# Performance work log

Hardware: AMD Instinct MI355X
Metric: run time of the kernel (lower is better)

The kernel has to match this reference:

```python
import jax, jax.numpy as jnp
import numpy as np

ATT_DIM = 2048
NUM_HEADS = 16
NUM_KV_GROUPS = 4
HEAD_DIM = 128
CONTEXT_LENGTH = 2048
ROPE_BASE = 10000.0
GROUP_SIZE = NUM_HEADS // NUM_KV_GROUPS
BATCH = 2


def _precompute_rope_sin(context_length, head_dim, rope_base):
    # thetas over rope_dim = head_dim // 2, exponent uses rope_dim (as in source)
    rope_dim = head_dim // 2
    j = jnp.arange(rope_dim, dtype=jnp.float32)
    thetas = 1.0 / rope_base ** (2.0 * j / rope_dim)
    positions = jnp.arange(context_length, dtype=jnp.float32)
    angles = positions[:, None] * thetas[None, :]          # [CD, HD//2]
    angles = jnp.concatenate([angles, angles], axis=-1)    # [CD, HD]
    return jnp.sin(angles)                                  # cos is unused (see bug note)


def _apply_rope(qk, sin):
    # FAITHFUL to source bug: in compute_rope, `cos` is overwritten with the
    # broadcast `sin`, so the returned value is qk*sin + qk_2*sin.
    hd = qk.shape[-1]
    qkr = qk[..., : hd // 2]
    qki = qk[..., hd // 2 :]
    qk2 = jnp.concatenate([-qki, qkr], axis=-1)
    sin_b = sin[None, None, : qk.shape[2], :]
    return qk * sin_b + qk2 * sin  # second term broadcasts full-length sin (requires cd==context_length)


def setup_inputs() -> dict:
    key = jax.random.key(0)
    ks = jax.random.split(key, 6)
    s = 0.02
    x = jax.random.normal(ks[0], (BATCH, CONTEXT_LENGTH, ATT_DIM), dtype=jnp.float32)
    Wq = jax.random.normal(ks[1], (ATT_DIM, HEAD_DIM * NUM_HEADS), dtype=jnp.float32) * s
    Wk = jax.random.normal(ks[2], (ATT_DIM, HEAD_DIM * NUM_KV_GROUPS), dtype=jnp.float32) * s
    Wv = jax.random.normal(ks[3], (ATT_DIM, HEAD_DIM * NUM_KV_GROUPS), dtype=jnp.float32) * s
    Wo = jax.random.normal(ks[4], (HEAD_DIM * NUM_HEADS, HEAD_DIM * NUM_HEADS), dtype=jnp.float32) * s
    bo = jax.random.normal(ks[5], (HEAD_DIM * NUM_HEADS,), dtype=jnp.float32) * s
    return {"x": x, "Wq": Wq, "Wk": Wk, "Wv": Wv, "Wo": Wo, "bo": bo}


def reference(x, Wq, Wk, Wv, Wo, bo):
    bd, cd, ed = x.shape
    sin = _precompute_rope_sin(CONTEXT_LENGTH, HEAD_DIM, ROPE_BASE)

    q = (x @ Wq).reshape(bd, cd, NUM_HEADS, HEAD_DIM).transpose(0, 2, 1, 3)      # [B,NH,CD,HD]
    k = (x @ Wk).reshape(bd, cd, NUM_KV_GROUPS, HEAD_DIM).transpose(0, 2, 1, 3)  # [B,Nkv,CD,HD]
    v = (x @ Wv).reshape(bd, cd, NUM_KV_GROUPS, HEAD_DIM).transpose(0, 2, 1, 3)

    q = _apply_rope(q, sin)
    k = _apply_rope(k, sin)

    k = jnp.repeat(k, GROUP_SIZE, axis=1)  # [B,NH,CD,HD]
    v = jnp.repeat(v, GROUP_SIZE, axis=1)

    a = jnp.einsum("bhqd,bhkd->bhqk", q, k)  # [B,NH,CD,CD]
    causal = jnp.triu(jnp.ones((cd, cd), dtype=bool), k=1)
    a = jnp.where(causal[None, None], -jnp.inf, a)
    a = jax.nn.softmax(a / jnp.sqrt(jnp.float32(HEAD_DIM)), axis=-1)

    y = jnp.einsum("bhqk,bhkd->bhqd", a, v)                # [B,NH,CD,HD]
    y = y.transpose(0, 2, 1, 3).reshape(bd, cd, HEAD_DIM * NUM_HEADS)
    return y @ Wo + bo
```

## Files before the change

### kernel.cpp

```cpp
#include <hip/hip_runtime.h>
#include <hip/hip_bf16.h>
#include <cstdint>
#include <cstddef>

#define BATCH 2
#define CTX 2048
#define EMB 2048
#define NH 16
#define NG 4
#define HD 128
#define NQK (EMB + 2*NG*HD)
#define MROWS (BATCH*CTX)

typedef __bf16 bf16x8 __attribute__((ext_vector_type(8)));
typedef float  f32x4  __attribute__((ext_vector_type(4)));
typedef float  f32x16 __attribute__((ext_vector_type(16)));

__device__ __forceinline__ ushort f2bf(float f) {
    uint32_t u = __float_as_uint(f);
    u += 0x7FFFu + ((u >> 16) & 1u);
    return (ushort)(u >> 16);
}

__device__ __forceinline__ float bf2f(ushort u) {
    return __uint_as_float((uint32_t)u << 16);
}

__device__ __forceinline__ uint32_t packbf(float a, float b) {
    ushort lo = __builtin_bit_cast(ushort, (__bf16)a);
    ushort hi = __builtin_bit_cast(ushort, (__bf16)b);
    return (uint32_t)lo | ((uint32_t)hi << 16);
}

__device__ __forceinline__ bf16x8 mkfrag(uint32_t a, uint32_t b, uint32_t c, uint32_t d) {
    union { uint32_t u[4]; bf16x8 v; } z;
    z.u[0] = a; z.u[1] = b; z.u[2] = c; z.u[3] = d;
    return z.v;
}

__device__ __forceinline__ void gload_lds16(const void* g, void* l) {
    __builtin_amdgcn_global_load_lds((const __attribute__((address_space(1))) void*)g,
                                     (__attribute__((address_space(3))) void*)l, 16, 0, 0);
}

__global__ __launch_bounds__(256) void k_sintab(float* __restrict__ sintab) {
    int t = blockIdx.x * 256 + threadIdx.x;
    int j = t & 63, p = t >> 6;
    float theta = 1.0f / powf(10000.0f, (float)(2 * j) / 64.0f);
    sintab[t] = sinf((float)p * theta);
}

__global__ __launch_bounds__(256) void k_cvt(const float4* __restrict__ src, ushort4* __restrict__ dst) {
    int i = blockIdx.x * 256 + threadIdx.x;
    float4 v = src[i];
    ushort4 o;
    o.x = f2bf(v.x); o.y = f2bf(v.y); o.z = f2bf(v.z); o.w = f2bf(v.w);
    dst[i] = o;
}

__global__ __launch_bounds__(256) void k_transpose_cvt(const float* __restrict__ src, int src_ld,
                                                       ushort* __restrict__ dst, int dst_ld) {
    __shared__ float tile[32][33];
    int tx = threadIdx.x, ty = threadIdx.y;
    int c0 = blockIdx.x * 32, r0 = blockIdx.y * 32;
    #pragma unroll
    for (int i = 0; i < 4; ++i)
        tile[ty + i*8][tx] = src[(size_t)(r0 + ty + i*8) * src_ld + c0 + tx];
    __syncthreads();
    #pragma unroll
    for (int i = 0; i < 4; ++i)
        dst[(size_t)(c0 + ty + i*8) * dst_ld + r0 + tx] = f2bf(tile[tx][ty + i*8]);
}

__global__ __launch_bounds__(256) void k_rope_f(const ushort* __restrict__ qkv,
                                                const float* __restrict__ sintab,
                                                ushort* __restrict__ Qf, ushort* __restrict__ Kf,
                                                float qs) {
    int t = blockIdx.x * 256 + threadIdx.x;
    int j = t & 63;
    int rest = t >> 6;
    int pos = rest & (CTX - 1);
    int rest2 = rest >> 11;
    int u = rest2 % (NH + NG);
    int b = rest2 / (NH + NG);
    const ushort* base;
    ushort* dst;
    float scale;
    if (u < NH) {
        base = qkv + (size_t)(b * CTX + pos) * NQK + u * HD;
        dst = Qf + (size_t)((b * NH + u) * 64 + (pos >> 5)) * 4096;
        scale = qs;
    } else {
        int g = u - NH;
        base = qkv + (size_t)(b * CTX + pos) * NQK + EMB + g * HD;
        dst = Kf + (size_t)((b * NG + g) * 64 + (pos >> 5)) * 4096;
        scale = 1.0f;
    }
    float a  = bf2f(base[j]);
    float bb = bf2f(base[j + 64]);
    float sv = sintab[pos * 64 + j] * scale;
    size_t idx0 = (size_t)(j >> 4) * 512 + ((j >> 3) & 1) * 256 + (pos & 31) * 8 + (j & 7);
    dst[idx0]        = f2bf((a - bb) * sv);
    dst[idx0 + 2048] = f2bf((bb + a) * sv);
}

__global__ __launch_bounds__(256) void k_vfrag(const ushort* __restrict__ qkvb, ushort* __restrict__ Vf) {
    int lane = threadIdx.x;
    int dt   = threadIdx.y;
    int step = blockIdx.x;
    int bg   = blockIdx.y;
    int b = bg >> 2, g = bg & 3;
    int ln = lane & 31, hi = lane >> 5;
    int col = EMB + NG*HD + g*HD + dt*32 + ln;
    #pragma unroll
    for (int ks = 0; ks < 2; ++ks) {
        int pos0 = step*32 + ks*16 + hi*8;
        ushort v[8];
        #pragma unroll
        for (int e = 0; e < 8; ++e)
            v[e] = qkvb[(size_t)(b*CTX + pos0 + e) * NQK + col];
        union { uint32_t u[4]; bf16x8 bv; } z;
        z.u[0] = (uint32_t)v[0] | ((uint32_t)v[1] << 16);
        z.u[1] = (uint32_t)v[2] | ((uint32_t)v[3] << 16);
        z.u[2] = (uint32_t)v[4] | ((uint32_t)v[5] << 16);
        z.u[3] = (uint32_t)v[6] | ((uint32_t)v[7] << 16);
        *(bf16x8*)(Vf + ((size_t)(bg*64 + step)*8 + dt*2 + ks) * 512 + lane*8) = z.bv;
    }
}

template<bool BF16OUT>
__global__ __launch_bounds__(256) void k_gemm_bt(const ushort* __restrict__ A, const ushort* __restrict__ Bt,
                                                 void* __restrict__ Cv, int M, int N, int K,
                                                 const float* __restrict__ bias) {
    __shared__ __align__(16) ushort As[2][128 * 32];
    __shared__ __align__(16) ushort Bs[2][128 * 32];
    int tid = threadIdx.x;
    int lane = tid & 63;
    int wave = tid >> 6;
    int wr = wave >> 1, wc = wave & 1;
    int m0 = blockIdx.y * 128, n0 = blockIdx.x * 128;
    int lr = lane & 15, lg = lane >> 4;

    f32x4 acc[4][4] = {};

    int arow = lane >> 2;
    int kpart = (lane & 3) * 8;

    int nsteps = K >> 5;

    #pragma unroll
    for (int s = 0; s < 2; ++s) {
        int c = wave * 2 + s;
        gload_lds16(A  + (size_t)(m0 + c*16 + arow) * K + kpart, &As[0][c * 512]);
        gload_lds16(Bt + (size_t)(n0 + c*16 + arow) * K + kpart, &Bs[0][c * 512]);
    }
    __syncthreads();

    for (int t = 0; t < nsteps; ++t) {
        int cur = t & 1;
        if (t + 1 < nsteps) {
            int k1 = (t + 1) << 5;
            #pragma unroll
            for (int s = 0; s < 2; ++s) {
                int c = wave * 2 + s;
                gload_lds16(A  + (size_t)(m0 + c*16 + arow) * K + k1 + kpart, &As[cur ^ 1][c * 512]);
                gload_lds16(Bt + (size_t)(n0 + c*16 + arow) * K + k1 + kpart, &Bs[cur ^ 1][c * 512]);
            }
        }
        bf16x8 af[4], bfr[4];
        #pragma unroll
        for (int mt = 0; mt < 4; ++mt)
            af[mt] = *(const bf16x8*)&As[cur][(wr*64 + mt*16 + lr) * 32 + lg * 8];
        #pragma unroll
        for (int nt = 0; nt < 4; ++nt)
            bfr[nt] = *(const bf16x8*)&Bs[cur][(wc*64 + nt*16 + lr) * 32 + lg * 8];
        #pragma unroll
        for (int mt = 0; mt < 4; ++mt)
            #pragma unroll
            for (int nt = 0; nt < 4; ++nt)
                acc[mt][nt] = __builtin_amdgcn_mfma_f32_16x16x32_bf16(af[mt], bfr[nt], acc[mt][nt], 0, 0, 0);
        __syncthreads();
    }

    #pragma unroll
    for (int mt = 0; mt < 4; ++mt) {
        #pragma unroll
        for (int nt = 0; nt < 4; ++nt) {
            int col = n0 + wc*64 + nt*16 + lr;
            float bv = bias ? bias[col] : 0.0f;
            #pragma unroll
            for (int r = 0; r < 4; ++r) {
                int row = m0 + wr*64 + mt*16 + lg*4 + r;
                float v = acc[mt][nt][r] + bv;
                if constexpr (BF16OUT)
                    ((ushort*)Cv)[(size_t)row * N + col] = f2bf(v);
                else
                    ((float*)Cv)[(size_t)row * N + col] = v;
            }
        }
    }
}

__global__ __launch_bounds__(128) void k_attn12(const ushort* __restrict__ Qf, const ushort* __restrict__ Kf,
                                                const ushort* __restrict__ Vf, ushort* __restrict__ y) {
    __shared__ __align__(16) char smem[16640];
    char*  Qs  = smem;
    float* sOd = (float*)smem;
    float* sl  = (float*)(smem + 16384);

    int lane = threadIdx.x & 63;
    int w    = threadIdx.x >> 6;
    int B  = blockIdx.x;
    int bg = B & 7;
    int within = B >> 3;
    int t  = 63 - (within >> 2);
    int hh = within & 3;
    int b = bg >> 2, g = bg & 3, h = g * 4 + hh;
    int ln = lane & 31, hi = lane >> 5;
    int q0 = t * 32;

    {
        const ushort* qf_g = Qf + ((size_t)((b*NH + h) * 64 + t)) * 4096;
        int tid = threadIdx.x;
        #pragma unroll
        for (int it = 0; it < 4; ++it)
            gload_lds16(qf_g + (it*128 + tid) * 8, Qs + it*2048 + w*1024);
    }
    __syncthreads();

    const ushort* kfb = Kf + (size_t)bg * 64 * 4096 + lane * 8;
    const ushort* vfb = Vf + (size_t)bg * 64 * 4096 + lane * 8;
    const char*   qsl = Qs + lane * 16;

    f32x16 od[4] = {};
    float lsum = 0.0f;

    auto step = [&](int si, bool diag) {
        const ushort* kp = kfb + (size_t)si * 4096;
        const ushort* vp = vfb + (size_t)si * 4096;
        f32x16 st = {};
        #pragma unroll
        for (int s = 0; s < 8; ++s) {
            bf16x8 kf = *(const bf16x8*)(kp + s * 512);
            bf16x8 qf = *(const bf16x8*)(qsl + s * 1024);
            st = __builtin_amdgcn_mfma_f32_32x32x16_bf16(kf, qf, st, 0, 0, 0);
        }

        if (diag) {
            #pragma unroll
            for (int r = 0; r < 16; ++r) {
                int kl = (r & 3) + 8*(r >> 2) + 4*hi;
                if (kl > ln) st[r] = -1e30f;
            }
        }
        #pragma unroll
        for (int r = 0; r < 16; ++r) st[r] = exp2f(st[r]);
        float s8[8];
        #pragma unroll
        for (int r = 0; r < 8; ++r) s8[r] = st[r] + st[r+8];
        #pragma unroll
        for (int r = 0; r < 4; ++r) s8[r] = s8[r] + s8[r+4];
        float ls = (s8[0] + s8[1]) + (s8[2] + s8[3]);
        lsum += ls + __shfl_xor(ls, 32, 64);

        #pragma unroll
        for (int ks = 0; ks < 2; ++ks) {
            uint32_t w0 = packbf(st[8*ks+0], st[8*ks+1]);
            uint32_t w1 = packbf(st[8*ks+2], st[8*ks+3]);
            uint32_t w2 = packbf(st[8*ks+4], st[8*ks+5]);
            uint32_t w3 = packbf(st[8*ks+6], st[8*ks+7]);
            uint32_t x0 = (uint32_t)__shfl_xor((int)w0, 32, 64);
            uint32_t x1 = (uint32_t)__shfl_xor((int)w1, 32, 64);
            uint32_t x2 = (uint32_t)__shfl_xor((int)w2, 32, 64);
            uint32_t x3 = (uint32_t)__shfl_xor((int)w3, 32, 64);
            bf16x8 pa = hi ? mkfrag(x2, x3, w2, w3) : mkfrag(w0, w1, x0, x1);
            #pragma unroll
            for (int dt = 0; dt < 4; ++dt) {
                bf16x8 vf = *(const bf16x8*)(vp + (dt*2 + ks) * 512);
                od[dt] = __builtin_amdgcn_mfma_f32_32x32x16_bf16(pa, vf, od[dt], 0, 0, 0);
            }
        }
    };

    for (int si = w; si < t; si += 2) step(si, false);
    if ((t & 1) == w) step(t, true);

    __syncthreads();
    if (w == 1) {
        #pragma unroll
        for (int r = 0; r < 16; ++r) {
            int ri = (r & 3) + 8*(r >> 2) + 4*hi;
            #pragma unroll
            for (int dt = 0; dt < 4; ++dt) sOd[ri*128 + dt*32 + ln] = od[dt][r];
        }
        if (hi == 0) sl[ln] = lsum;
    }
    __syncthreads();
    if (w == 0) {
        float inv = 1.0f / (lsum + sl[ln]);
        #pragma unroll
        for (int r = 0; r < 16; ++r) {
            int ri = (r & 3) + 8*(r >> 2) + 4*hi;
            float ivr = __shfl(inv, ri, 64);
            int row = q0 + ri;
            #pragma unroll
            for (int dt = 0; dt < 4; ++dt) {
                float v = (od[dt][r] + sOd[ri*128 + dt*32 + ln]) * ivr;
                y[((size_t)(b*CTX + row)) * (NH*HD) + h*HD + dt*32 + ln] = f2bf(v);
            }
        }
    }
}

#define SIN_OFF   ((size_t)0)
#define XB_OFF    ((size_t)524288)
#define WT_OFF    ((size_t)17301504)
#define WOT_OFF   ((size_t)29884416)
#define QKV_OFF   ((size_t)38273024)
#define QB_OFF    ((size_t)88604672)
#define KB_OFF    ((size_t)105381888)
#define VT_OFF    ((size_t)109576192)
#define YB_OFF    ((size_t)113770496)

extern "C" void kernel_launch(void* const* d_in, const int* in_sizes, int n_in,
                              void* d_out, int out_size, void* d_ws, size_t ws_size,
                              hipStream_t stream) {
    const float* x  = (const float*)d_in[0];
    const float* Wq = (const float*)d_in[1];
    const float* Wk = (const float*)d_in[2];
    const float* Wv = (const float*)d_in[3];
    const float* Wo = (const float*)d_in[4];
    const float* bo = (const float*)d_in[5];
    float* out = (float*)d_out;
    char* ws = (char*)d_ws;

    float*  sintab = (float*)(ws + SIN_OFF);
    ushort* xb     = (ushort*)(ws + XB_OFF);
    ushort* Wt     = (ushort*)(ws + WT_OFF);
    ushort* Wot    = (ushort*)(ws + WOT_OFF);
    ushort* QKVb   = (ushort*)(ws + QKV_OFF);
    ushort* Qf     = (ushort*)(ws + QB_OFF);
    ushort* Kf     = (ushort*)(ws + KB_OFF);
    ushort* Vf     = (ushort*)(ws + VT_OFF);
    ushort* yb     = (ushort*)(ws + YB_OFF);

    k_sintab<<<512, 256, 0, stream>>>(sintab);
    k_cvt<<<(MROWS * EMB / 4) / 256, 256, 0, stream>>>((const float4*)x, (ushort4*)xb);
    dim3 tb(32, 8);
    k_transpose_cvt<<<dim3(EMB/32, EMB/32), tb, 0, stream>>>(Wq, EMB, Wt, EMB);
    k_transpose_cvt<<<dim3((NG*HD)/32, EMB/32), tb, 0, stream>>>(Wk, NG*HD, Wt + (size_t)EMB * EMB, EMB);
    k_transpose_cvt<<<dim3((NG*HD)/32, EMB/32), tb, 0, stream>>>(Wv, NG*HD, Wt + (size_t)(EMB + NG*HD) * EMB, EMB);
    k_transpose_cvt<<<dim3(EMB/32, EMB/32), tb, 0, stream>>>(Wo, EMB, Wot, EMB);
    k_gemm_bt<true><<<dim3(NQK/128, MROWS/128), 256, 0, stream>>>(xb, Wt, QKVb, MROWS, NQK, EMB, nullptr);
    const float qscale = 0.08838834764831845f * 1.4426950408889634f;
    k_rope_f<<<(BATCH*(NH+NG)*CTX*64)/256, 256, 0, stream>>>(QKVb, sintab, Qf, Kf, qscale);
    k_vfrag<<<dim3(64, BATCH*NG), dim3(64, 4), 0, stream>>>(QKVb, Vf);
    k_attn12<<<2048, 128, 0, stream>>>(Qf, Kf, Vf, yb);
    k_gemm_bt<false><<<dim3(EMB/128, MROWS/128), 256, 0, stream>>>(yb, Wot, out, MROWS, EMB, EMB, bo);
}
```

Before: 223.0 us.

## Fuse RoPE and V fragment layout into QKV GEMM epilogue, merge weight transposes

The QKV projection GEMM now stages its output tile in LDS and writes it directly as RoPE-applied Q/K fragments or reordered V fragments. This removes the intermediate QKV buffer along with the separate rope and vfrag kernels and their global-memory round trip. The four weight transpose launches are merged into one 3D-grid launch that exits early for out-of-range tiles. In exchange, the GEMM epilogue gets longer and the kernel uses more shared memory.

New measurement: 210.8 us. -5.5%, faster.

```diff
diff --git a/kernel.cpp b/kernel.cpp
--- a/kernel.cpp
+++ b/kernel.cpp
@@ -58,11 +58,19 @@
     dst[i] = o;
 }
 
-__global__ __launch_bounds__(256) void k_transpose_cvt(const float* __restrict__ src, int src_ld,
-                                                       ushort* __restrict__ dst, int dst_ld) {
+__global__ __launch_bounds__(256) void k_transpose_all(const float* __restrict__ Wq, const float* __restrict__ Wk,
+                                                       const float* __restrict__ Wv, const float* __restrict__ Wo,
+                                                       ushort* __restrict__ Wt, ushort* __restrict__ Wot) {
     __shared__ float tile[32][33];
+    int z = blockIdx.z;
+    const float* src; ushort* dst; int src_ld, dst_ld, ncols;
+    if (z == 0)      { src = Wq; dst = Wt;                              src_ld = EMB;   dst_ld = EMB; ncols = EMB; }
+    else if (z == 1) { src = Wk; dst = Wt + (size_t)EMB * EMB;          src_ld = NG*HD; dst_ld = EMB; ncols = NG*HD; }
+    else if (z == 2) { src = Wv; dst = Wt + (size_t)(EMB + NG*HD) * EMB; src_ld = NG*HD; dst_ld = EMB; ncols = NG*HD; }
+    else             { src = Wo; dst = Wot;                             src_ld = EMB;   dst_ld = EMB; ncols = EMB; }
+    int c0 = blockIdx.x * 32, r0 = blockIdx.y * 32;
+    if (c0 >= ncols) return;
     int tx = threadIdx.x, ty = threadIdx.y;
-    int c0 = blockIdx.x * 32, r0 = blockIdx.y * 32;
     #pragma unroll
     for (int i = 0; i < 4; ++i)
         tile[ty + i*8][tx] = src[(size_t)(r0 + ty + i*8) * src_ld + c0 + tx];
@@ -72,65 +80,119 @@
         dst[(size_t)(c0 + ty + i*8) * dst_ld + r0 + tx] = f2bf(tile[tx][ty + i*8]);
 }
 
-__global__ __launch_bounds__(256) void k_rope_f(const ushort* __restrict__ qkv,
-                                                const float* __restrict__ sintab,
-                                                ushort* __restrict__ Qf, ushort* __restrict__ Kf,
-                                                float qs) {
-    int t = blockIdx.x * 256 + threadIdx.x;
-    int j = t & 63;
-    int rest = t >> 6;
-    int pos = rest & (CTX - 1);
-    int rest2 = rest >> 11;
-    int u = rest2 % (NH + NG);
-    int b = rest2 / (NH + NG);
-    const ushort* base;
-    ushort* dst;
-    float scale;
-    if (u < NH) {
-        base = qkv + (size_t)(b * CTX + pos) * NQK + u * HD;
-        dst = Qf + (size_t)((b * NH + u) * 64 + (pos >> 5)) * 4096;
-        scale = qs;
+__global__ __launch_bounds__(256) void k_gemm_qkv(const ushort* __restrict__ A, const ushort* __restrict__ Bt,
+                                                  const float* __restrict__ sintab,
+                                                  ushort* __restrict__ Qf, ushort* __restrict__ Kf,
+                                                  ushort* __restrict__ Vf, float qscale) {
+    __shared__ __align__(16) char smem[33792];
+    int tid = threadIdx.x;
+    int lane = tid & 63;
+    int wave = tid >> 6;
+    int wr = wave >> 1, wc = wave & 1;
+    int m0 = blockIdx.y * 128, n0 = blockIdx.x * 128;
+    int lr = lane & 15, lg = lane >> 4;
+
+    f32x4 acc[4][4] = {};
+
+    int arow = lane >> 2;
+    int kpart = (lane & 3) * 8;
+
+    ushort* As = (ushort*)smem;
+    ushort* Bs = (ushort*)(smem + 16384);
+
+    #pragma unroll
+    for (int s = 0; s < 2; ++s) {
+        int c = wave * 2 + s;
+        gload_lds16(A  + (size_t)(m0 + c*16 + arow) * EMB + kpart, &As[c * 512]);
+        gload_lds16(Bt + (size_t)(n0 + c*16 + arow) * EMB + kpart, &Bs[c * 512]);
+    }
+    __syncthreads();
+
+    for (int t = 0; t < EMB/32; ++t) {
+        int cur = t & 1;
+        if (t + 1 < EMB/32) {
+            int k1 = (t + 1) << 5;
+            #pragma unroll
+            for (int s = 0; s < 2; ++s) {
+                int c = wave * 2 + s;
+                gload_lds16(A  + (size_t)(m0 + c*16 + arow) * EMB + k1 + kpart, &As[(cur^1)*4096 + c*512]);
+                gload_lds16(Bt + (size_t)(n0 + c*16 + arow) * EMB + k1 + kpart, &Bs[(cur^1)*4096 + c*512]);
+            }
+        }
+        bf16x8 af[4], bfr[4];
+        #pragma unroll
+        for (int mt = 0; mt < 4; ++mt)
+            af[mt] = *(const bf16x8*)&As[cur*4096 + (wr*64 + mt*16 + lr) * 32 + lg * 8];
+        #pragma unroll
+        for (int nt = 0; nt < 4; ++nt)
+            bfr[nt] = *(const bf16x8*)&Bs[cur*4096 + (wc*64 + nt*16 + lr) * 32 + lg * 8];
+        #pragma unroll
+        for (int mt = 0; mt < 4; ++mt)
+            #pragma unroll
+            for (int nt = 0; nt < 4; ++nt)
+                acc[mt][nt] = __builtin_amdgcn_mfma_f32_16x16x32_bf16(af[mt], bfr[nt], acc[mt][nt], 0, 0, 0);
+        __syncthreads();
+    }
+
+    ushort* clds = (ushort*)smem;
+    #pragma unroll
+    for (int mt = 0; mt < 4; ++mt) {
+        #pragma unroll
+        for (int nt = 0; nt < 4; ++nt) {
+            int col = wc*64 + nt*16 + lr;
+            int row = wr*64 + mt*16 + lg*4;
+            ushort4 pk;
+            pk.x = f2bf(acc[mt][nt][0]); pk.y = f2bf(acc[mt][nt][1]);
+            pk.z = f2bf(acc[mt][nt][2]); pk.w = f2bf(acc[mt][nt][3]);
+            *(ushort4*)&clds[col*132 + row] = pk;
+        }
+    }
+    __syncthreads();
+
+    int xt = blockIdx.x;
+    int b = m0 >> 11;
+    int pos0 = m0 & 2047;
+
+    if (xt < 20) {
+        int j = tid & 63;
+        int rgrp = tid >> 6;
+        ushort* dstb;
+        float scl;
+        if (xt < 16) { dstb = Qf + (size_t)((b*NH + xt) * 64) * 4096;      scl = qscale; }
+        else         { dstb = Kf + (size_t)((b*NG + (xt-16)) * 64) * 4096; scl = 1.0f;   }
+        #pragma unroll 4
+        for (int it = 0; it < 32; ++it) {
+            int row = rgrp + it*4;
+            int pos = pos0 + row;
+            float a  = bf2f(clds[j*132 + row]);
+            float bb = bf2f(clds[(j+64)*132 + row]);
+            float sv = sintab[pos*64 + j] * scl;
+            size_t idx = (size_t)(pos>>5)*4096 + (size_t)(j>>4)*512 + ((j>>3)&1)*256 + (pos&31)*8 + (j&7);
+            dstb[idx]        = f2bf((a - bb) * sv);
+            dstb[idx + 2048] = f2bf((bb + a) * sv);
+        }
     } else {
-        int g = u - NH;
-        base = qkv + (size_t)(b * CTX + pos) * NQK + EMB + g * HD;
-        dst = Kf + (size_t)((b * NG + g) * 64 + (pos >> 5)) * 4096;
-        scale = 1.0f;
-    }
-    float a  = bf2f(base[j]);
-    float bb = bf2f(base[j + 64]);
-    float sv = sintab[pos * 64 + j] * scale;
-    size_t idx0 = (size_t)(j >> 4) * 512 + ((j >> 3) & 1) * 256 + (pos & 31) * 8 + (j & 7);
-    dst[idx0]        = f2bf((a - bb) * sv);
-    dst[idx0 + 2048] = f2bf((bb + a) * sv);
-}
-
-__global__ __launch_bounds__(256) void k_vfrag(const ushort* __restrict__ qkvb, ushort* __restrict__ Vf) {
-    int lane = threadIdx.x;
-    int dt   = threadIdx.y;
-    int step = blockIdx.x;
-    int bg   = blockIdx.y;
-    int b = bg >> 2, g = bg & 3;
-    int ln = lane & 31, hi = lane >> 5;
-    int col = EMB + NG*HD + g*HD + dt*32 + ln;
-    #pragma unroll
-    for (int ks = 0; ks < 2; ++ks) {
-        int pos0 = step*32 + ks*16 + hi*8;
-        ushort v[8];
-        #pragma unroll
-        for (int e = 0; e < 8; ++e)
-            v[e] = qkvb[(size_t)(b*CTX + pos0 + e) * NQK + col];
-        union { uint32_t u[4]; bf16x8 bv; } z;
-        z.u[0] = (uint32_t)v[0] | ((uint32_t)v[1] << 16);
-        z.u[1] = (uint32_t)v[2] | ((uint32_t)v[3] << 16);
-        z.u[2] = (uint32_t)v[4] | ((uint32_t)v[5] << 16);
-        z.u[3] = (uint32_t)v[6] | ((uint32_t)v[7] << 16);
-        *(bf16x8*)(Vf + ((size_t)(bg*64 + step)*8 + dt*2 + ks) * 512 + lane*8) = z.bv;
-    }
-}
-
-template<bool BF16OUT>
+        int g = xt - 20;
+        int bg = b*NG + g;
+        int ln2 = tid & 31, hi2 = (tid >> 5) & 1, dt = tid >> 6;
+        int colc = dt*32 + ln2;
+        #pragma unroll
+        for (int stp = 0; stp < 4; ++stp) {
+            #pragma unroll
+            for (int ks = 0; ks < 2; ++ks) {
+                int rowb = stp*32 + ks*16 + hi2*8;
+                union { ushort4 q[2]; bf16x8 v; } z;
+                z.q[0] = *(ushort4*)&clds[colc*132 + rowb];
+                z.q[1] = *(ushort4*)&clds[colc*132 + rowb + 4];
+                int step_g = (pos0 >> 5) + stp;
+                *(bf16x8*)(Vf + ((size_t)(bg*64 + step_g)*8 + dt*2 + ks) * 512 + (tid & 63) * 8) = z.v;
+            }
+        }
+    }
+}
+
 __global__ __launch_bounds__(256) void k_gemm_bt(const ushort* __restrict__ A, const ushort* __restrict__ Bt,
-                                                 void* __restrict__ Cv, int M, int N, int K,
+                                                 float* __restrict__ C, int M, int N, int K,
                                                  const float* __restrict__ bias) {
     __shared__ __align__(16) ushort As[2][128 * 32];
     __shared__ __align__(16) ushort Bs[2][128 * 32];
@@ -191,11 +253,7 @@
             #pragma unroll
             for (int r = 0; r < 4; ++r) {
                 int row = m0 + wr*64 + mt*16 + lg*4 + r;
-                float v = acc[mt][nt][r] + bv;
-                if constexpr (BF16OUT)
-                    ((ushort*)Cv)[(size_t)row * N + col] = f2bf(v);
-                else
-                    ((float*)Cv)[(size_t)row * N + col] = v;
+                C[(size_t)row * N + col] = acc[mt][nt][r] + bv;
             }
         }
     }
@@ -316,7 +374,6 @@
 #define XB_OFF    ((size_t)524288)
 #define WT_OFF    ((size_t)17301504)
 #define WOT_OFF   ((size_t)29884416)
-#define QKV_OFF   ((size_t)38273024)
 #define QB_OFF    ((size_t)88604672)
 #define KB_OFF    ((size_t)105381888)
 #define VT_OFF    ((size_t)109576192)
@@ -338,23 +395,17 @@
     ushort* xb     = (ushort*)(ws + XB_OFF);
     ushort* Wt     = (ushort*)(ws + WT_OFF);
     ushort* Wot    = (ushort*)(ws + WOT_OFF);
-    ushort* QKVb   = (ushort*)(ws + QKV_OFF);
     ushort* Qf     = (ushort*)(ws + QB_OFF);
     ushort* Kf     = (ushort*)(ws + KB_OFF);
     ushort* Vf     = (ushort*)(ws + VT_OFF);
     ushort* yb     = (ushort*)(ws + YB_OFF);
 
+    const float qscale = 0.08838834764831845f * 1.4426950408889634f;
+
     k_sintab<<<512, 256, 0, stream>>>(sintab);
     k_cvt<<<(MROWS * EMB / 4) / 256, 256, 0, stream>>>((const float4*)x, (ushort4*)xb);
-    dim3 tb(32, 8);
-    k_transpose_cvt<<<dim3(EMB/32, EMB/32), tb, 0, stream>>>(Wq, EMB, Wt, EMB);
-    k_transpose_cvt<<<dim3((NG*HD)/32, EMB/32), tb, 0, stream>>>(Wk, NG*HD, Wt + (size_t)EMB * EMB, EMB);
-    k_transpose_cvt<<<dim3((NG*HD)/32, EMB/32), tb, 0, stream>>>(Wv, NG*HD, Wt + (size_t)(EMB + NG*HD) * EMB, EMB);
-    k_transpose_cvt<<<dim3(EMB/32, EMB/32), tb, 0, stream>>>(Wo, EMB, Wot, EMB);
-    k_gemm_bt<true><<<dim3(NQK/128, MROWS/128), 256, 0, stream>>>(xb, Wt, QKVb, MROWS, NQK, EMB, nullptr);
-    const float qscale = 0.08838834764831845f * 1.4426950408889634f;
-    k_rope_f<<<(BATCH*(NH+NG)*CTX*64)/256, 256, 0, stream>>>(QKVb, sintab, Qf, Kf, qscale);
-    k_vfrag<<<dim3(64, BATCH*NG), dim3(64, 4), 0, stream>>>(QKVb, Vf);
+    k_transpose_all<<<dim3(64, 64, 4), dim3(32, 8), 0, stream>>>(Wq, Wk, Wv, Wo, Wt, Wot);
+    k_gemm_qkv<<<dim3(NQK/128, MROWS/128), 256, 0, stream>>>(xb, Wt, sintab, Qf, Kf, Vf, qscale);
     k_attn12<<<2048, 128, 0, stream>>>(Qf, Kf, Vf, yb);
-    k_gemm_bt<false><<<dim3(EMB/128, MROWS/128), 256, 0, stream>>>(yb, Wot, out, MROWS, EMB, EMB, bo);
-}
+    k_gemm_bt<<<dim3(EMB/128, MROWS/128), 256, 0, stream>>>(yb, Wot, out, MROWS, EMB, EMB, bo);
+}
```
